# Kernel tuning notes

Hardware: AMD Instinct MI355X
Metric: run time of the kernel (lower is better)

Reference implementation:

```python
import jax, jax.numpy as jnp
import numpy as np
import math

CHANNELS = 512
N_HEADS = 8
K_CH = CHANNELS // N_HEADS            # 64 per-head dim
ROPE_D = int(K_CH * 0.5)              # 32 dims get RoPE, rest pass through
BASE = 10000


def _rope(x):
    # x: [b, h, t, dk]; rotate first ROPE_D dims (half-split style, matching the torch module)
    d = ROPE_D
    t = x.shape[2]
    theta = 1.0 / (BASE ** (jnp.arange(0, d, 2, dtype=jnp.float32) / d))      # [d/2]
    ang = jnp.arange(t, dtype=jnp.float32)[:, None] * theta[None, :]          # [t, d/2]
    ang = jnp.concatenate([ang, ang], axis=-1)                                # [t, d]
    cos = jnp.cos(ang)[None, None, :, :].astype(x.dtype)
    sin = jnp.sin(ang)[None, None, :, :].astype(x.dtype)
    x_rope, x_pass = x[..., :d], x[..., d:]
    neg_half = jnp.concatenate([-x_rope[..., d // 2:], x_rope[..., :d // 2]], axis=-1)
    return jnp.concatenate([x_rope * cos + neg_half * sin, x_pass], axis=-1)


def _split_heads(y):
    # [b, (h c), t] -> [b, h, t, c]
    b, _, t = y.shape
    return y.reshape(b, N_HEADS, K_CH, t).transpose(0, 1, 3, 2)


def setup_inputs() -> dict:
    key = jax.random.key(0)
    ks = jax.random.split(key, 10)
    B, T = 8, 1024
    w_scale = 1.0 / math.sqrt(CHANNELS)
    return {
        "x": jax.random.normal(ks[0], (B, CHANNELS, T), jnp.float32),
        "c": jax.random.normal(ks[1], (B, CHANNELS, T), jnp.float32),
        "Wq": jax.random.normal(ks[2], (CHANNELS, CHANNELS), jnp.float32) * w_scale,
        "bq": jax.random.normal(ks[3], (CHANNELS,), jnp.float32) * 0.02,
        "Wk": jax.random.normal(ks[4], (CHANNELS, CHANNELS), jnp.float32) * w_scale,
        "bk": jax.random.normal(ks[5], (CHANNELS,), jnp.float32) * 0.02,
        "Wv": jax.random.normal(ks[6], (CHANNELS, CHANNELS), jnp.float32) * w_scale,
        "bv": jax.random.normal(ks[7], (CHANNELS,), jnp.float32) * 0.02,
        "Wo": jax.random.normal(ks[8], (CHANNELS, CHANNELS), jnp.float32) * w_scale,
        "bo": jax.random.normal(ks[9], (CHANNELS,), jnp.float32) * 0.02,
    }


def reference(x, c, Wq, bq, Wk, bk, Wv, bv, Wo, bo):
    # 1x1 Conv1d == per-timestep linear over channels
    q = jnp.einsum('oc,bct->bot', Wq, x) + bq[None, :, None]
    k = jnp.einsum('oc,bct->bot', Wk, c) + bk[None, :, None]
    v = jnp.einsum('oc,bct->bot', Wv, c) + bv[None, :, None]

    q = _rope(_split_heads(q))            # [b,h,t,ck]
    k = _rope(_split_heads(k))            # [b,h,s,ck]
    v = _split_heads(v)                   # [b,h,s,ck]

    scale = 1.0 / math.sqrt(K_CH)
    scores = jnp.einsum('bhtc,bhsc->bhts', q, k) * scale
    p_attn = jax.nn.softmax(scores, axis=-1)       # dropout p=0 -> identity
    out = jnp.einsum('bhts,bhsc->bhtc', p_attn, v)

    b, _, t, _ = out.shape
    out = out.transpose(0, 1, 3, 2).reshape(b, CHANNELS, t)   # [b, (h c), t]
    return jnp.einsum('oc,bct->bot', Wo, out) + bo[None, :, None]
```

## Files before the change

### kernel.cpp

```cpp
#include <hip/hip_runtime.h>

typedef __bf16 bf16x8 __attribute__((ext_vector_type(8)));
typedef float  f32x4  __attribute__((ext_vector_type(4)));

__device__ __forceinline__ unsigned short f2bf(float f){
    union { float f; unsigned u; } v; v.f = f;
    v.u += 0x7fffu + ((v.u >> 16) & 1u);
    return (unsigned short)(v.u >> 16);
}
__device__ __forceinline__ void gl2lds16(const unsigned short* g, unsigned short* l){
    __builtin_amdgcn_global_load_lds(
        (const __attribute__((address_space(1))) void*)g,
        (__attribute__((address_space(3))) void*)l, 16, 0, 0);
}

__global__ __launch_bounds__(256) void transpose_cvt(const float* __restrict__ x, const float* __restrict__ c,
                                                     const float* __restrict__ w0, const float* __restrict__ w1,
                                                     const float* __restrict__ w2, const float* __restrict__ w3,
                                                     unsigned short* __restrict__ xt, unsigned short* __restrict__ ct,
                                                     unsigned short* __restrict__ o0, unsigned short* __restrict__ o1,
                                                     unsigned short* __restrict__ o2, unsigned short* __restrict__ o3){
    __shared__ float tile[64][72];
    const int z = blockIdx.z;
    if (z == 16){
        int fid = (blockIdx.x * 8 + blockIdx.y) * 256 + threadIdx.x;
        const float* in; unsigned short* out;
        switch (fid >> 13){
            case 0: in = w0; out = o0; break;
            case 1: in = w1; out = o1; break;
            case 2: in = w2; out = o2; break;
            default: in = w3; out = o3; break;
        }
        int off = (fid & 8191) * 32;
        #pragma unroll
        for (int j = 0; j < 8; j++){
            float4 v = *(const float4*)(in + off + j*4);
            ushort4 o; o.x = f2bf(v.x); o.y = f2bf(v.y); o.z = f2bf(v.z); o.w = f2bf(v.w);
            *(ushort4*)(out + off + j*4) = o;
        }
        return;
    }
    const float* in = (z < 8) ? x : c;
    unsigned short* out = (z < 8) ? xt : ct;
    const int b = z & 7;
    const int t0 = blockIdx.x * 64, c0 = blockIdx.y * 64;
    const int tid = threadIdx.x;
    {
        int r = tid >> 2, q = (tid & 3) * 16;
        const float* src = in + ((size_t)b * 512 + c0 + r) * 1024 + t0 + q;
        #pragma unroll
        for (int j = 0; j < 4; j++)
            *(float4*)&tile[r][q + j*4] = ((const float4*)src)[j];
    }
    __syncthreads();
    {
        int tr = tid >> 2, cj = (tid & 3) * 16;
        unsigned pw[8];
        #pragma unroll
        for (int j = 0; j < 8; j++){
            unsigned lo = f2bf(tile[cj + 2*j    ][tr]);
            unsigned hi = f2bf(tile[cj + 2*j + 1][tr]);
            pw[j] = lo | (hi << 16);
        }
        unsigned short* dst = out + ((size_t)b * 1024 + t0 + tr) * 512 + c0 + cj;
        uint4 q0 = {pw[0], pw[1], pw[2], pw[3]};
        uint4 q1 = {pw[4], pw[5], pw[6], pw[7]};
        ((uint4*)dst)[0] = q0;
        ((uint4*)dst)[1] = q1;
    }
}

__device__ __forceinline__ void gemm_mainloop(const unsigned short* __restrict__ A,
                                              const unsigned short* __restrict__ Bm,
                                              unsigned short* a_s, unsigned short* b_s,
                                              int m0, int n0, int tid, f32x4 acc[4][4]){
    const int wave = tid >> 6, lane = tid & 63;
    const int l15 = lane & 15, l4 = lane >> 4;
    const int mw = (wave >> 1) * 64, nw = (wave & 1) * 64;
    const int r8 = lane >> 3, c8l = lane & 7;
    const int csw = (c8l ^ r8) * 8;
    const int rp = l15 & 7;

    auto stage = [&](int k0, int buf){
        unsigned short* as = a_s + buf * (128*64);
        unsigned short* bs = b_s + buf * (128*64);
        #pragma unroll
        for (int i = 0; i < 4; i++){
            int rg = i * 4 + wave;
            int row = rg * 8 + r8;
            gl2lds16(A  + (size_t)(m0 + row) * 512 + k0 + csw, as + rg * 512);
            gl2lds16(Bm + (size_t)(n0 + row) * 512 + k0 + csw, bs + rg * 512);
        }
    };

    stage(0, 0);
    __syncthreads();

    for (int t = 0; t < 8; t++){
        const int buf = t & 1;
        if (t < 7) stage((t + 1) * 64, buf ^ 1);
        const unsigned short* as = a_s + buf * (128*64);
        const unsigned short* bs = b_s + buf * (128*64);
        #pragma unroll
        for (int kk = 0; kk < 2; kk++){
            bf16x8 af[4], bfr[4];
            #pragma unroll
            for (int mt = 0; mt < 4; mt++)
                af[mt] = *(const bf16x8*)&as[(mw + mt*16 + l15)*64 + (((kk*4) + l4) ^ rp)*8];
            #pragma unroll
            for (int ct = 0; ct < 4; ct++)
                bfr[ct] = *(const bf16x8*)&bs[(nw + ct*16 + l15)*64 + (((kk*4) + l4) ^ rp)*8];
            #pragma unroll
            for (int mt = 0; mt < 4; mt++)
                #pragma unroll
                for (int ct = 0; ct < 4; ct++)
                    acc[mt][ct] = __builtin_amdgcn_mfma_f32_16x16x32_bf16(
                        af[mt], bfr[ct], acc[mt][ct], 0, 0, 0);
        }
        __syncthreads();
    }
}

__global__ __launch_bounds__(256) void qkv_gemm(const unsigned short* __restrict__ xt,
                                                const unsigned short* __restrict__ ct,
                                                const unsigned short* __restrict__ wq,
                                                const unsigned short* __restrict__ wk,
                                                const unsigned short* __restrict__ wv,
                                                const float* __restrict__ bq_,
                                                const float* __restrict__ bk_,
                                                const float* __restrict__ bv_,
                                                unsigned short* __restrict__ qt,
                                                unsigned short* __restrict__ kt,
                                                unsigned short* __restrict__ vct){
    __shared__ unsigned short a_s[2*128*64];
    __shared__ unsigned short b_s[2*128*64];
    const int z = blockIdx.y;
    const int xr = blockIdx.x;
    const int bid = (xr & 7) * 32 + (xr >> 3);
    const unsigned short *A, *Bm;
    int m0, n0;
    if (z == 0){ A = xt; Bm = wq; m0 = (bid >> 2)*128; n0 = (bid & 3)*128; }
    else if (z == 1){ A = ct; Bm = wk; m0 = (bid >> 2)*128; n0 = (bid & 3)*128; }
    else { A = wv; Bm = ct; m0 = (bid & 3)*128; n0 = (bid >> 2)*128; }
    const int tid = threadIdx.x;
    const int wave = tid >> 6, lane = tid & 63;
    const int l15 = lane & 15, l4 = lane >> 4;
    const int mw = (wave >> 1) * 64, nw = (wave & 1) * 64;
    const f32x4 vzero = {0.f, 0.f, 0.f, 0.f};
    f32x4 acc[4][4];
    #pragma unroll
    for (int i = 0; i < 4; i++)
        #pragma unroll
        for (int j = 0; j < 4; j++) acc[i][j] = vzero;

    gemm_mainloop(A, Bm, a_s, b_s, m0, n0, tid, acc);

    if (z < 2){
        unsigned short* out = (z == 0) ? qt : kt;
        const float* bias = (z == 0) ? bq_ : bk_;
        const float osc = (z == 0) ? 0.1803368801111137f : 1.0f;
        float bv4[4];
        #pragma unroll
        for (int ct2 = 0; ct2 < 4; ct2++) bv4[ct2] = bias[n0 + nw + ct2*16 + l15];
        const float theta = __powf(10000.0f, -(float)l15 * (1.0f / 16.0f));
        #pragma unroll
        for (int mt = 0; mt < 4; mt++){
            #pragma unroll
            for (int rr = 0; rr < 4; rr++){
                int row = m0 + mw + mt*16 + l4*4 + rr;
                int t = row & 1023;
                float v[4];
                #pragma unroll
                for (int ct2 = 0; ct2 < 4; ct2++) v[ct2] = acc[mt][ct2][rr] + bv4[ct2];
                float sn, cn;
                __sincosf((float)t * theta, &sn, &cn);
                float r0 = v[0] * cn - v[1] * sn;
                float r1 = v[1] * cn + v[0] * sn;
                v[0] = r0; v[1] = r1;
                #pragma unroll
                for (int ct2 = 0; ct2 < 4; ct2++)
                    out[(size_t)row * 512 + n0 + nw + ct2*16 + l15] = f2bf(v[ct2] * osc);
            }
        }
    } else {
        #pragma unroll
        for (int mt = 0; mt < 4; mt++){
            #pragma unroll
            for (int rr = 0; rr < 4; rr++){
                int row = m0 + mw + mt*16 + l4*4 + rr;
                float bb = bv_[row];
                #pragma unroll
                for (int ct2 = 0; ct2 < 4; ct2++){
                    int n = n0 + nw + ct2*16 + l15;
                    size_t oaddr = (size_t)(n >> 10) * 524288 + (size_t)row * 1024 + (n & 1023);
                    vct[oaddr] = f2bf(acc[mt][ct2][rr] + bb);
                }
            }
        }
    }
}

__global__ __launch_bounds__(256) void gemm_o(const unsigned short* __restrict__ wo,
                                              const unsigned short* __restrict__ attnT,
                                              const float* __restrict__ bo,
                                              float* __restrict__ out){
    __shared__ unsigned short a_s[2*64*64];
    __shared__ unsigned short b_s[2*128*64];
    const int m0 = blockIdx.x * 64, n0 = blockIdx.y * 128;
    const int tid = threadIdx.x;
    const int wave = tid >> 6, lane = tid & 63;
    const int l15 = lane & 15, l4 = lane >> 4;
    const int nw = wave * 32;
    const int r8 = lane >> 3, c8l = lane & 7;
    const int csw = (c8l ^ r8) * 8;
    const int rp = l15 & 7;
    const f32x4 vzero = {0.f, 0.f, 0.f, 0.f};
    f32x4 acc[4][2];
    #pragma unroll
    for (int i = 0; i < 4; i++){ acc[i][0] = vzero; acc[i][1] = vzero; }

    auto stage = [&](int k0, int buf){
        unsigned short* as = a_s + buf * (64*64);
        unsigned short* bs = b_s + buf * (128*64);
        #pragma unroll
        for (int i = 0; i < 2; i++){
            int rg = wave * 2 + i;
            gl2lds16(wo + (size_t)(m0 + rg*8 + r8) * 512 + k0 + csw, as + rg * 512);
        }
        #pragma unroll
        for (int i = 0; i < 4; i++){
            int rg = wave * 4 + i;
            gl2lds16(attnT + (size_t)(n0 + rg*8 + r8) * 512 + k0 + csw, bs + rg * 512);
        }
    };

    stage(0, 0);
    __syncthreads();

    for (int t = 0; t < 8; t++){
        const int buf = t & 1;
        if (t < 7) stage((t + 1) * 64, buf ^ 1);
        const unsigned short* as = a_s + buf * (64*64);
        const unsigned short* bs = b_s + buf * (128*64);
        #pragma unroll
        for (int kk = 0; kk < 2; kk++){
            bf16x8 af[4], bfr[2];
            #pragma unroll
            for (int mt = 0; mt < 4; mt++)
                af[mt] = *(const bf16x8*)&as[(mt*16 + l15)*64 + (((kk*4) + l4) ^ rp)*8];
            #pragma unroll
            for (int ct = 0; ct < 2; ct++)
                bfr[ct] = *(const bf16x8*)&bs[(nw + ct*16 + l15)*64 + (((kk*4) + l4) ^ rp)*8];
            #pragma unroll
            for (int mt = 0; mt < 4; mt++)
                #pragma unroll
                for (int ct = 0; ct < 2; ct++)
                    acc[mt][ct] = __builtin_amdgcn_mfma_f32_16x16x32_bf16(
                        af[mt], bfr[ct], acc[mt][ct], 0, 0, 0);
        }
        __syncthreads();
    }

    #pragma unroll
    for (int mt = 0; mt < 4; mt++){
        #pragma unroll
        for (int rr = 0; rr < 4; rr++){
            int row = m0 + mt*16 + l4*4 + rr;
            float bb = bo[row];
            #pragma unroll
            for (int ct2 = 0; ct2 < 2; ct2++){
                int n = n0 + nw + ct2*16 + l15;
                size_t oaddr = (size_t)(n >> 10) * 524288 + (size_t)row * 1024 + (n & 1023);
                out[oaddr] = acc[mt][ct2][rr] + bb;
            }
        }
    }
}

__global__ __launch_bounds__(256, 2) void flash_attn(const unsigned short* __restrict__ qt,
                                                     const unsigned short* __restrict__ kt,
                                                     const unsigned short* __restrict__ vct,
                                                     unsigned short* __restrict__ attnT){
    __shared__ unsigned short k_s[2][64*64];
    __shared__ unsigned short v_s[2][64*64];
    const int bhq = blockIdx.x;
    const int bh = bhq & 63, b = bh >> 3, h = bh & 7;
    const int q0 = (bhq >> 6) * 128;
    const int tid = threadIdx.x, wave = tid >> 6, lane = tid & 63;
    const int l15 = lane & 15, l4 = lane >> 4;
    const int r8 = lane >> 3, c8l = lane & 7;
    const int csw = (c8l ^ r8) * 8;
    const int rp = l15 & 7;
    const f32x4 vzero = {0.f, 0.f, 0.f, 0.f};
    const unsigned short* kbase = kt  + (size_t)(b*1024)*512 + h*64;
    const unsigned short* vbase = vct + (size_t)(b*512 + h*64)*1024;

    bf16x8 qf[2][2];
    #pragma unroll
    for (int st = 0; st < 2; st++)
        #pragma unroll
        for (int kh = 0; kh < 2; kh++)
            qf[st][kh] = *(const bf16x8*)(qt + (size_t)(b*1024 + q0 + wave*32 + st*16 + l15)*512
                                             + h*64 + kh*32 + l4*8);
    f32x4 o_acc[2][4], l_acc[2];
    #pragma unroll
    for (int st = 0; st < 2; st++){
        l_acc[st] = vzero;
        #pragma unroll
        for (int dt = 0; dt < 4; dt++) o_acc[st][dt] = vzero;
    }
    const __bf16 one_bf = (__bf16)1.0f;
    const bf16x8 ones = {one_bf, one_bf, one_bf, one_bf, one_bf, one_bf, one_bf, one_bf};

    auto stage = [&](int tile, int buf){
        const int s0n = tile * 64;
        #pragma unroll
        for (int i = 0; i < 2; i++){
            int rg = i * 4 + wave;
            int row = rg * 8 + r8;
            gl2lds16(kbase + (size_t)(s0n + row)*512 + csw, &k_s[buf][rg*512]);
            gl2lds16(vbase + (size_t)row*1024 + s0n + csw, &v_s[buf][rg*512]);
        }
    };
    stage(0, 0);
    __syncthreads();

    const int voff0 = (l4 & 1) * 4;
    for (int it = 0; it < 16; ++it){
        const int cur = it & 1;
        if (it < 15) stage(it + 1, cur ^ 1);
        bf16x8 kf[2][4];
        #pragma unroll
        for (int kh = 0; kh < 2; kh++)
            #pragma unroll
            for (int ct = 0; ct < 4; ct++)
                kf[kh][ct] = *(const bf16x8*)&k_s[cur][(ct*16 + l15)*64 + ((kh*4 + l4) ^ rp)*8];
        union bfv { bf16x8 v; uint2 u[2]; };
        bfv vfp[2][4];
        #pragma unroll
        for (int c2 = 0; c2 < 2; c2++)
            #pragma unroll
            for (int dt = 0; dt < 4; dt++){
                const int base = (dt*16 + l15)*64;
                const int ch0 = ((c2*4 +     (l4 >> 1)) ^ rp)*8 + voff0;
                const int ch1 = ((c2*4 + 2 + (l4 >> 1)) ^ rp)*8 + voff0;
                vfp[c2][dt].u[0] = *(const uint2*)&v_s[cur][base + ch0];
                vfp[c2][dt].u[1] = *(const uint2*)&v_s[cur][base + ch1];
            }
        #pragma unroll
        for (int st = 0; st < 2; st++){
            f32x4 sa[4];
            #pragma unroll
            for (int ct = 0; ct < 4; ct++) sa[ct] = vzero;
            #pragma unroll
            for (int kh = 0; kh < 2; kh++)
                #pragma unroll
                for (int ct = 0; ct < 4; ct++)
                    sa[ct] = __builtin_amdgcn_mfma_f32_16x16x32_bf16(kf[kh][ct], qf[st][kh], sa[ct], 0, 0, 0);
            #pragma unroll
            for (int ct = 0; ct < 4; ct++)
                #pragma unroll
                for (int rr = 0; rr < 4; rr++)
                    sa[ct][rr] = exp2f(sa[ct][rr]);
            bf16x8 ap[2];
            #pragma unroll
            for (int c2 = 0; c2 < 2; c2++){
                union { unsigned u[4]; bf16x8 v; } pw;
                #pragma unroll
                for (int c1 = 0; c1 < 2; c1++){
                    union { float f; unsigned u; } x0, x1, x2, x3;
                    x0.f = sa[2*c2+c1][0]; x1.f = sa[2*c2+c1][1];
                    x2.f = sa[2*c2+c1][2]; x3.f = sa[2*c2+c1][3];
                    pw.u[c1*2+0] = (x0.u >> 16) | (x1.u & 0xffff0000u);
                    pw.u[c1*2+1] = (x2.u >> 16) | (x3.u & 0xffff0000u);
                }
                ap[c2] = pw.v;
            }
            l_acc[st] = __builtin_amdgcn_mfma_f32_16x16x32_bf16(ap[0], ones, l_acc[st], 0, 0, 0);
            l_acc[st] = __builtin_amdgcn_mfma_f32_16x16x32_bf16(ap[1], ones, l_acc[st], 0, 0, 0);
            #pragma unroll
            for (int dt = 0; dt < 4; dt++){
                o_acc[st][dt] = __builtin_amdgcn_mfma_f32_16x16x32_bf16(ap[0], vfp[0][dt].v, o_acc[st][dt], 0, 0, 0);
                o_acc[st][dt] = __builtin_amdgcn_mfma_f32_16x16x32_bf16(ap[1], vfp[1][dt].v, o_acc[st][dt], 0, 0, 0);
            }
        }
        __syncthreads();
    }
    #pragma unroll
    for (int st = 0; st < 2; st++){
        float rl[4];
        #pragma unroll
        for (int rr = 0; rr < 4; rr++) rl[rr] = __builtin_amdgcn_rcpf(l_acc[st][rr]);
        #pragma unroll
        for (int dt = 0; dt < 4; dt++)
            #pragma unroll
            for (int rr = 0; rr < 4; rr++){
                int row = q0 + wave*32 + st*16 + l4*4 + rr;
                attnT[(size_t)(b*1024 + row)*512 + h*64 + dt*16 + l15] = f2bf(o_acc[st][dt][rr] * rl[rr]);
            }
    }
}

extern "C" void kernel_launch(void* const* d_in, const int* in_sizes, int n_in,
                              void* d_out, int out_size, void* d_ws, size_t ws_size,
                              hipStream_t stream){
    const float* x  = (const float*)d_in[0];
    const float* c  = (const float*)d_in[1];
    const float* Wq = (const float*)d_in[2];
    const float* bq = (const float*)d_in[3];
    const float* Wk = (const float*)d_in[4];
    const float* bk = (const float*)d_in[5];
    const float* Wv = (const float*)d_in[6];
    const float* bv = (const float*)d_in[7];
    const float* Wo = (const float*)d_in[8];
    const float* bo = (const float*)d_in[9];

    unsigned short* wq_b = (unsigned short*)d_ws;
    unsigned short* wk_b = wq_b + 262144;
    unsigned short* wv_b = wk_b + 262144;
    unsigned short* wo_b = wv_b + 262144;
    unsigned short* xt   = wo_b + 262144;
    unsigned short* ct   = xt  + 4194304;
    unsigned short* qt   = ct  + 4194304;
    unsigned short* kt   = qt  + 4194304;
    unsigned short* vct  = kt  + 4194304;
    unsigned short* attnT = xt;

    transpose_cvt<<<dim3(16, 8, 17), 256, 0, stream>>>(x, c, Wq, Wk, Wv, Wo,
                                                       xt, ct, wq_b, wk_b, wv_b, wo_b);
    qkv_gemm<<<dim3(256, 3), 256, 0, stream>>>(xt, ct, wq_b, wk_b, wv_b, bq, bk, bv, qt, kt, vct);
    flash_attn<<<dim3(512), 256, 0, stream>>>(qt, kt, vct, attnT);
    gemm_o<<<dim3(8, 64), 256, 0, stream>>>(wo_b, attnT, bo, (float*)d_out);
}
```

Measured before the change: 166.3 us.

## Halve flash-attention query tile per block and swizzle transpose LDS tile

The flash attention kernel now gives each wave 16 query rows instead of 32, doubling the grid to 1024 blocks and raising the launch-bounds occupancy hint to 4 blocks per CU. The goal is more parallelism and latency hiding across CUs. In exchange, each K/V tile loaded into shared memory is reused by half as many queries, which doubles K/V global traffic. Separately, the transpose kernel XOR-swizzles its shared-memory tile columns to cut bank conflicts on the column-wise reads.

```diff
diff --git a/kernel.cpp b/kernel.cpp
--- a/kernel.cpp
+++ b/kernel.cpp
@@ -47,19 +47,21 @@
     const int tid = threadIdx.x;
     {
         int r = tid >> 2, q = (tid & 3) * 16;
+        int qs = q ^ (((r >> 4) & 3) << 4);
         const float* src = in + ((size_t)b * 512 + c0 + r) * 1024 + t0 + q;
         #pragma unroll
         for (int j = 0; j < 4; j++)
-            *(float4*)&tile[r][q + j*4] = ((const float4*)src)[j];
+            *(float4*)&tile[r][qs + j*4] = ((const float4*)src)[j];
     }
     __syncthreads();
     {
         int tr = tid >> 2, cj = (tid & 3) * 16;
+        const int fsw = ((cj >> 4) & 3) << 4;
         unsigned pw[8];
         #pragma unroll
         for (int j = 0; j < 8; j++){
-            unsigned lo = f2bf(tile[cj + 2*j    ][tr]);
-            unsigned hi = f2bf(tile[cj + 2*j + 1][tr]);
+            unsigned lo = f2bf(tile[cj + 2*j    ][tr ^ fsw]);
+            unsigned hi = f2bf(tile[cj + 2*j + 1][tr ^ fsw]);
             pw[j] = lo | (hi << 16);
         }
         unsigned short* dst = out + ((size_t)b * 1024 + t0 + tr) * 512 + c0 + cj;
@@ -277,7 +279,7 @@
     }
 }
 
-__global__ __launch_bounds__(256, 2) void flash_attn(const unsigned short* __restrict__ qt,
+__global__ __launch_bounds__(256, 4) void flash_attn(const unsigned short* __restrict__ qt,
                                                      const unsigned short* __restrict__ kt,
                                                      const unsigned short* __restrict__ vct,
                                                      unsigned short* __restrict__ attnT){
@@ -285,7 +287,7 @@
     __shared__ unsigned short v_s[2][64*64];
     const int bhq = blockIdx.x;
     const int bh = bhq & 63, b = bh >> 3, h = bh & 7;
-    const int q0 = (bhq >> 6) * 128;
+    const int q0 = (bhq >> 6) * 64;
     const int tid = threadIdx.x, wave = tid >> 6, lane = tid & 63;
     const int l15 = lane & 15, l4 = lane >> 4;
     const int r8 = lane >> 3, c8l = lane & 7;
@@ -295,20 +297,14 @@
     const unsigned short* kbase = kt  + (size_t)(b*1024)*512 + h*64;
     const unsigned short* vbase = vct + (size_t)(b*512 + h*64)*1024;
 
-    bf16x8 qf[2][2];
+    bf16x8 qf[2];
     #pragma unroll
-    for (int st = 0; st < 2; st++)
-        #pragma unroll
-        for (int kh = 0; kh < 2; kh++)
-            qf[st][kh] = *(const bf16x8*)(qt + (size_t)(b*1024 + q0 + wave*32 + st*16 + l15)*512
-                                             + h*64 + kh*32 + l4*8);
-    f32x4 o_acc[2][4], l_acc[2];
+    for (int kh = 0; kh < 2; kh++)
+        qf[kh] = *(const bf16x8*)(qt + (size_t)(b*1024 + q0 + wave*16 + l15)*512
+                                     + h*64 + kh*32 + l4*8);
+    f32x4 o_acc[4], l_acc = vzero;
     #pragma unroll
-    for (int st = 0; st < 2; st++){
-        l_acc[st] = vzero;
-        #pragma unroll
-        for (int dt = 0; dt < 4; dt++) o_acc[st][dt] = vzero;
-    }
+    for (int dt = 0; dt < 4; dt++) o_acc[dt] = vzero;
     const __bf16 one_bf = (__bf16)1.0f;
     const bf16x8 ones = {one_bf, one_bf, one_bf, one_bf, one_bf, one_bf, one_bf, one_bf};
 
@@ -347,56 +343,52 @@
                 vfp[c2][dt].u[0] = *(const uint2*)&v_s[cur][base + ch0];
                 vfp[c2][dt].u[1] = *(const uint2*)&v_s[cur][base + ch1];
             }
-        #pragma unroll
-        for (int st = 0; st < 2; st++){
-            f32x4 sa[4];
-            #pragma unroll
-            for (int ct = 0; ct < 4; ct++) sa[ct] = vzero;
-            #pragma unroll
-            for (int kh = 0; kh < 2; kh++)
-                #pragma unroll
-                for (int ct = 0; ct < 4; ct++)
-                    sa[ct] = __builtin_amdgcn_mfma_f32_16x16x32_bf16(kf[kh][ct], qf[st][kh], sa[ct], 0, 0, 0);
+        f32x4 sa[4];
+        #pragma unroll
+        for (int ct = 0; ct < 4; ct++) sa[ct] = vzero;
+        #pragma unroll
+        for (int kh = 0; kh < 2; kh++)
             #pragma unroll
             for (int ct = 0; ct < 4; ct++)
-                #pragma unroll
-                for (int rr = 0; rr < 4; rr++)
-                    sa[ct][rr] = exp2f(sa[ct][rr]);
-            bf16x8 ap[2];
-            #pragma unroll
-            for (int c2 = 0; c2 < 2; c2++){
-                union { unsigned u[4]; bf16x8 v; } pw;
-                #pragma unroll
-                for (int c1 = 0; c1 < 2; c1++){
-                    union { float f; unsigned u; } x0, x1, x2, x3;
-                    x0.f = sa[2*c2+c1][0]; x1.f = sa[2*c2+c1][1];
-                    x2.f = sa[2*c2+c1][2]; x3.f = sa[2*c2+c1][3];
-                    pw.u[c1*2+0] = (x0.u >> 16) | (x1.u & 0xffff0000u);
-                    pw.u[c1*2+1] = (x2.u >> 16) | (x3.u & 0xffff0000u);
-                }
-                ap[c2] = pw.v;
-            }
-            l_acc[st] = __builtin_amdgcn_mfma_f32_16x16x32_bf16(ap[0], ones, l_acc[st], 0, 0, 0);
-            l_acc[st] = __builtin_amdgcn_mfma_f32_16x16x32_bf16(ap[1], ones, l_acc[st], 0, 0, 0);
-            #pragma unroll
-            for (int dt = 0; dt < 4; dt++){
-                o_acc[st][dt] = __builtin_amdgcn_mfma_f32_16x16x32_bf16(ap[0], vfp[0][dt].v, o_acc[st][dt], 0, 0, 0);
-                o_acc[st][dt] = __builtin_amdgcn_mfma_f32_16x16x32_bf16(ap[1], vfp[1][dt].v, o_acc[st][dt], 0, 0, 0);
-            }
+                sa[ct] = __builtin_amdgcn_mfma_f32_16x16x32_bf16(kf[kh][ct], qf[kh], sa[ct], 0, 0, 0);
+        #pragma unroll
+        for (int ct = 0; ct < 4; ct++)
+            #pragma unroll
+            for (int rr = 0; rr < 4; rr++)
+                sa[ct][rr] = exp2f(sa[ct][rr]);
+        bf16x8 ap[2];
+        #pragma unroll
+        for (int c2 = 0; c2 < 2; c2++){
+            union { unsigned u[4]; bf16x8 v; } pw;
+            #pragma unroll
+            for (int c1 = 0; c1 < 2; c1++){
+                union { float f; unsigned u; } x0, x1, x2, x3;
+                x0.f = sa[2*c2+c1][0]; x1.f = sa[2*c2+c1][1];
+                x2.f = sa[2*c2+c1][2]; x3.f = sa[2*c2+c1][3];
+                pw.u[c1*2+0] = (x0.u >> 16) | (x1.u & 0xffff0000u);
+                pw.u[c1*2+1] = (x2.u >> 16) | (x3.u & 0xffff0000u);
+            }
+            ap[c2] = pw.v;
+        }
+        l_acc = __builtin_amdgcn_mfma_f32_16x16x32_bf16(ap[0], ones, l_acc, 0, 0, 0);
+        l_acc = __builtin_amdgcn_mfma_f32_16x16x32_bf16(ap[1], ones, l_acc, 0, 0, 0);
+        #pragma unroll
+        for (int dt = 0; dt < 4; dt++){
+            o_acc[dt] = __builtin_amdgcn_mfma_f32_16x16x32_bf16(ap[0], vfp[0][dt].v, o_acc[dt], 0, 0, 0);
+            o_acc[dt] = __builtin_amdgcn_mfma_f32_16x16x32_bf16(ap[1], vfp[1][dt].v, o_acc[dt], 0, 0, 0);
         }
         __syncthreads();
     }
-    #pragma unroll
-    for (int st = 0; st < 2; st++){
+    {
         float rl[4];
         #pragma unroll
-        for (int rr = 0; rr < 4; rr++) rl[rr] = __builtin_amdgcn_rcpf(l_acc[st][rr]);
+        for (int rr = 0; rr < 4; rr++) rl[rr] = __builtin_amdgcn_rcpf(l_acc[rr]);
         #pragma unroll
         for (int dt = 0; dt < 4; dt++)
             #pragma unroll
             for (int rr = 0; rr < 4; rr++){
-                int row = q0 + wave*32 + st*16 + l4*4 + rr;
-                attnT[(size_t)(b*1024 + row)*512 + h*64 + dt*16 + l15] = f2bf(o_acc[st][dt][rr] * rl[rr]);
+                int row = q0 + wave*16 + l4*4 + rr;
+                attnT[(size_t)(b*1024 + row)*512 + h*64 + dt*16 + l15] = f2bf(o_acc[dt][rr] * rl[rr]);
             }
     }
 }
@@ -429,6 +421,6 @@
     transpose_cvt<<<dim3(16, 8, 17), 256, 0, stream>>>(x, c, Wq, Wk, Wv, Wo,
                                                        xt, ct, wq_b, wk_b, wv_b, wo_b);
     qkv_gemm<<<dim3(256, 3), 256, 0, stream>>>(xt, ct, wq_b, wk_b, wv_b, bq, bk, bv, qt, kt, vct);
-    flash_attn<<<dim3(512), 256, 0, stream>>>(qt, kt, vct, attnT);
+    flash_attn<<<dim3(1024), 256, 0, stream>>>(qt, kt, vct, attnT);
     gemm_o<<<dim3(8, 64), 256, 0, stream>>>(wo_b, attnT, bo, (float*)d_out);
 }
```

After: 168.2 us. About the same (+1.1%).
